# Optimization experiments

Hardware: AMD Instinct MI355X
Metric: run time of the kernel (lower is better)

Reference implementation:

```python
import jax, jax.numpy as jnp
import numpy as np

SEQ, B, N, H, OUT, K, L = 32, 1024, 19, 128, 1, 2, 2


def setup_inputs() -> dict:
    key = jax.random.key(0)
    ks = jax.random.split(key, 16)
    s = lambda i, shape, scale=1.0: (jax.random.normal(ks[i], shape, jnp.float32) * scale)
    return {
        "inputs": s(0, (SEQ, B, N, OUT)),
        "initial_hidden_state": s(1, (L, B, N * H)),
        "support": s(2, (N, N)) * (1.0 / np.sqrt(N)),
        "W_gate0": s(3, (3 * (OUT + H), 2 * H)) * 0.05,
        "b_gate0": s(4, (2 * H,)) * 0.05,
        "W_cand0": s(5, (3 * (OUT + H), H)) * 0.05,
        "b_cand0": s(6, (H,)) * 0.05,
        "W_gate1": s(7, (3 * (H + H), 2 * H)) * 0.05,
        "b_gate1": s(8, (2 * H,)) * 0.05,
        "W_cand1": s(9, (3 * (H + H), H)) * 0.05,
        "b_cand1": s(10, (H,)) * 0.05,
        "W_proj": s(11, (H, OUT)) * 0.05,
        "b_proj": s(12, (OUT,)) * 0.05,
    }


def reference(inputs, initial_hidden_state, support, W_gate0, b_gate0, W_cand0,
              b_cand0, W_gate1, b_gate1, W_cand1, b_cand1, W_proj, b_proj):
    seq_len, batch = inputs.shape[0], inputs.shape[1]
    h0 = initial_hidden_state.reshape(L, batch, N, H)

    def gconv(x, W, b):
        # Chebyshev diffusion: x0, T1=S@x0, T2=2*S@T1-x0 (K=2, 1 support)
        x0 = x
        x1 = jnp.einsum('mn,bnf->bmf', support, x0)
        feats = [x0, x1]
        for _ in range(K - 1):
            x2 = 2.0 * jnp.einsum('mn,bnf->bmf', support, x1) - x0
            feats.append(x2)
            x0, x1 = x1, x2
        X = jnp.concatenate(feats, axis=-1)  # (B, N, F*num_matrices)
        return jnp.einsum('bnf,fo->bno', X, W) + b

    def cell(x_in, h, Wg, bg, Wc, bc):
        ru = jax.nn.sigmoid(gconv(jnp.concatenate([x_in, h], axis=-1), Wg, bg))
        r, u = jnp.split(ru, 2, axis=-1)
        c = jnp.tanh(gconv(jnp.concatenate([x_in, r * h], axis=-1), Wc, bc))
        return u * h + (1.0 - u) * c

    layer_params = [(W_gate0, b_gate0, W_cand0, b_cand0),
                    (W_gate1, b_gate1, W_cand1, b_cand1)]

    def step(carry, _):
        h, cur = carry
        new_h = []
        x = cur
        for i, (Wg, bg, Wc, bc) in enumerate(layer_params):
            x = cell(x, h[i], Wg, bg, Wc, bc)
            new_h.append(x)
        proj = jnp.einsum('bnh,ho->bno', x, W_proj) + b_proj  # (B, N, OUT)
        out_t = proj.reshape(batch, N * OUT)
        return (jnp.stack(new_h, axis=0), proj), out_t

    go = jnp.zeros((batch, N, OUT), inputs.dtype)
    (_, _), outputs = jax.lax.scan(step, (h0, go), None, length=seq_len)
    return outputs  # (seq_len, batch, N*OUT)
```

## Files before the change

kernel.cpp:

```cpp
#include <hip/hip_runtime.h>
#include <hip/hip_bf16.h>
#include <math.h>

#define SEQ   32
#define BATCH 1024
#define NN    19
#define HH    128
#define NB    4
#define MR    (NB*NN)
#define SAS   264
#define HS    132
#define UTS   72
#define NBLK  (BATCH/NB)
#define NT    512

#define OFF_G0 0
#define OFF_C0 122880
#define OFF_G1 184320
#define OFF_C1 380928
#define WTOT   479232

__device__ unsigned short g_wall[WTOT];
__device__ unsigned short g_tg[2048];

typedef __attribute__((ext_vector_type(8))) short  bf16x8;
typedef __attribute__((ext_vector_type(4))) float  f32x4;

__device__ __forceinline__ unsigned short f2bf(float v) {
    __hip_bfloat16 b = __float2bfloat16(v);
    return *reinterpret_cast<unsigned short*>(&b);
}
__device__ __forceinline__ float bf2f(unsigned short u) {
    unsigned int x = ((unsigned int)u) << 16;
    return __uint_as_float(x);
}
__device__ __forceinline__ float hload(const unsigned short* p) { return bf2f(*p); }
__device__ __forceinline__ float hload(const float* p)          { return *p; }
__device__ __forceinline__ void  hstore(unsigned short* p, float v) { *p = f2bf(v); }
__device__ __forceinline__ void  hstore(float* p, float v)          { *p = v; }

__global__ __launch_bounds__(256) void wconv_kernel(
    const float* __restrict__ W, int F, int O, int KP, int off)
{
    int idx = blockIdx.x*256 + threadIdx.x;
    int total = 3*O*KP;
    if (idx >= total) return;
    int j   = idx / (O*KP);
    int r   = idx - j*(O*KP);
    int col = r / KP;
    int k   = r - col*KP;
    float v = (k < F) ? W[(size_t)(j*F + k)*O + col] : 0.f;
    g_wall[off + idx] = f2bf(v);
}

__global__ __launch_bounds__(256) void tprime_kernel(const float* __restrict__ S)
{
    __shared__ float sS[NN*NN], sS2[NN*NN];
    int tid = threadIdx.x;
    for (int i = tid; i < NN*NN; i += 256) sS[i] = S[i];
    __syncthreads();
    for (int i = tid; i < NN*NN; i += 256) {
        int m = i/NN, n = i - m*NN;
        float a = 0.f;
        for (int k = 0; k < NN; ++k) a += sS[m*NN+k]*sS[k*NN+n];
        sS2[i] = a;
    }
    __syncthreads();
    for (int i = tid; i < 32*64; i += 256) {
        int m = i >> 6, k = i & 63;
        float v = 0.f;
        if (m < NN && k < 3*NN) {
            int j = k / NN, n = k - j*NN;
            float eye = (m == n) ? 1.f : 0.f;
            if (j == 0)      v = eye;
            else if (j == 1) v = sS[m*NN+n];
            else             v = 2.f*sS2[m*NN+n] - eye;
        }
        g_tg[i] = f2bf(v);
    }
}

#define LDS_BYTES 159664

template<int KS, int NTC, bool GATE, int XW, typename HT>
__device__ __forceinline__ void gconv_phase(
    const unsigned short* __restrict__ BT,
    const float* __restrict__ bias,
    HT* hL,
    unsigned short* sA,
    unsigned short* ub,
    unsigned short* UtW,
    int lane, int w)
{
    constexpr int OC = NTC*128;
    constexpr int KP = KS*32;
    const int r16 = lane & 15, quad = lane >> 4;
    const int sgo = w * (NTC*16);

    const unsigned short* lanep = BT + (size_t)(sgo + r16)*KP + quad*8;

    f32x4 acc[3][5][NTC];
    #pragma unroll
    for (int j = 0; j < 3; ++j)
        #pragma unroll
        for (int mt = 0; mt < 5; ++mt)
            #pragma unroll
            for (int nt = 0; nt < NTC; ++nt) acc[j][mt][nt] = (f32x4)0.f;

    bf16x8 ring[2][3][NTC];
    #pragma unroll
    for (int j = 0; j < 3; ++j)
        #pragma unroll
        for (int nt = 0; nt < NTC; ++nt) {
            ring[0][j][nt] = *(const bf16x8*)(lanep + (size_t)(j*OC + nt*16)*KP);
            if (KS > 1)
                ring[1][j][nt] = *(const bf16x8*)(lanep + (size_t)(j*OC + nt*16)*KP + 32);
        }

    #pragma unroll
    for (int ks = 0; ks < KS; ++ks) {
        #pragma unroll
        for (int mt = 0; mt < 5; ++mt) {
            bf16x8 af = *(const bf16x8*)&sA[(mt*16 + r16)*SAS + ks*32 + quad*8];
            #pragma unroll
            for (int j = 0; j < 3; ++j)
                #pragma unroll
                for (int nt = 0; nt < NTC; ++nt)
                    acc[j][mt][nt] = __builtin_amdgcn_mfma_f32_16x16x32_bf16(
                        af, ring[ks & 1][j][nt], acc[j][mt][nt], 0, 0, 0);
        }
        if (ks + 2 < KS) {
            #pragma unroll
            for (int j = 0; j < 3; ++j)
                #pragma unroll
                for (int nt = 0; nt < NTC; ++nt)
                    ring[ks & 1][j][nt] = *(const bf16x8*)(lanep +
                        (size_t)(j*OC + nt*16)*KP + (ks + 2)*32);
        }
    }

    if (GATE) __syncthreads();

    float bv[NTC];
    #pragma unroll
    for (int nt = 0; nt < NTC; ++nt) bv[nt] = bias[sgo + nt*16 + r16];

    bf16x8 tp[2][2];
    #pragma unroll
    for (int mt2 = 0; mt2 < 2; ++mt2)
        #pragma unroll
        for (int kk = 0; kk < 2; ++kk)
            tp[mt2][kk] = *(const bf16x8*)&g_tg[(mt2*16 + r16)*64 + kk*32 + quad*8];

    for (int b = 0; b < NB; ++b) {
        #pragma unroll
        for (int j = 0; j < 3; ++j)
            #pragma unroll
            for (int mt = 0; mt < 5; ++mt)
                #pragma unroll
                for (int reg = 0; reg < 4; ++reg) {
                    int gm = mt*16 + quad*4 + reg;
                    int n  = gm - b*NN;
                    if (n >= 0 && n < NN) {
                        #pragma unroll
                        for (int nt = 0; nt < NTC; ++nt)
                            UtW[(nt*16 + r16)*UTS + j*NN + n] =
                                f2bf(acc[j][mt][nt][reg]);
                    }
                }
        f32x4 y[2][NTC];
        #pragma unroll
        for (int a = 0; a < 2; ++a)
            #pragma unroll
            for (int c = 0; c < NTC; ++c) y[a][c] = (f32x4)0.f;
        #pragma unroll
        for (int kk = 0; kk < 2; ++kk)
            #pragma unroll
            for (int nt = 0; nt < NTC; ++nt) {
                bf16x8 uf = *(const bf16x8*)&UtW[(nt*16 + r16)*UTS + kk*32 + quad*8];
                y[0][nt] = __builtin_amdgcn_mfma_f32_16x16x32_bf16(
                    tp[0][kk], uf, y[0][nt], 0, 0, 0);
                y[1][nt] = __builtin_amdgcn_mfma_f32_16x16x32_bf16(
                    tp[1][kk], uf, y[1][nt], 0, 0, 0);
            }
        #pragma unroll
        for (int mt2 = 0; mt2 < 2; ++mt2)
            #pragma unroll
            for (int nt = 0; nt < NTC; ++nt)
                #pragma unroll
                for (int reg = 0; reg < 4; ++reg) {
                    int m = mt2*16 + quad*4 + reg;
                    if (m < NN) {
                        int o = sgo + nt*16 + r16;
                        float v = y[mt2][nt][reg] + bv[nt];
                        int row = b*NN + m;
                        if (GATE) {
                            float sg_ = 1.f/(1.f + __expf(-v));
                            if (o < HH)
                                sA[row*SAS + XW + o] =
                                    f2bf(sg_ * hload(&hL[row*HS + o]));
                            else
                                ub[row*HS + (o-HH)] = f2bf(sg_);
                        } else {
                            float c  = 2.f/(1.f + __expf(-2.f*v)) - 1.f;
                            float u  = bf2f(ub[row*HS + o]);
                            float ho = hload(&hL[row*HS + o]);
                            hstore(&hL[row*HS + o], u*ho + (1.f - u)*c);
                        }
                    }
                }
    }
}

__global__ __launch_bounds__(NT, 2) void dcgru_persistent(
    const float* __restrict__ ihs,
    const float* __restrict__ bg0, const float* __restrict__ bc0,
    const float* __restrict__ bg1, const float* __restrict__ bc1,
    const float* __restrict__ Wp, const float* __restrict__ bp,
    float* __restrict__ out)
{
    extern __shared__ char smem[];
    unsigned short* h0    = (unsigned short*)smem;
    float*          h1    = (float*)(smem + 20064);
    unsigned short* sA    = (unsigned short*)(smem + 60192);
    unsigned short* ub    = (unsigned short*)(smem + 102432);
    unsigned short* Ut    = (unsigned short*)(smem + 122496);
    float*          xprev = (float*)(smem + 159360);

    const int tid  = threadIdx.x;
    const int lane = tid & 63;
    const int w    = tid >> 6;
    const int bb   = blockIdx.x * NB;
    unsigned short* UtW = Ut + w*32*UTS;

    const unsigned short* BTg0 = g_wall + OFF_G0;
    const unsigned short* BTc0 = g_wall + OFF_C0;
    const unsigned short* BTg1 = g_wall + OFF_G1;
    const unsigned short* BTc1 = g_wall + OFF_C1;

    for (int i = tid; i < MR*HH; i += NT) {
        int row = i >> 7, f = i & 127;
        h0[row*HS + f] = f2bf(ihs[(size_t)bb*2432 + i]);
        h1[row*HS + f] = ihs[(size_t)(BATCH + bb)*2432 + i];
    }
    for (int i = tid; i < MR; i += NT) xprev[i] = 0.f;
    for (int i = lane; i < 32*UTS; i += 64) UtW[i] = 0;

    const float wp0 = Wp[lane], wp1 = Wp[64 + lane], bpv = bp[0];
    __syncthreads();

    for (int t = 0; t < SEQ; ++t) {
        for (int idx = tid; idx < MR*160; idx += NT) {
            int row = idx/160, c = idx - row*160;
            unsigned short v;
            if (c == 0)       v = f2bf(xprev[row]);
            else if (c <= HH) v = h0[row*HS + (c-1)];
            else              v = 0;
            sA[row*SAS + c] = v;
        }
        __syncthreads();
        gconv_phase<5,2,true ,1>(BTg0, bg0, h0, sA, ub, UtW, lane, w);
        __syncthreads();
        gconv_phase<5,1,false,1>(BTc0, bc0, h0, sA, ub, UtW, lane, w);
        __syncthreads();

        for (int idx = tid; idx < MR*256; idx += NT) {
            int row = idx >> 8, c = idx & 255;
            sA[row*SAS + c] = (c < HH) ? h0[row*HS + c]
                                       : f2bf(h1[row*HS + (c-HH)]);
        }
        __syncthreads();
        gconv_phase<8,2,true ,HH>(BTg1, bg1, h1, sA, ub, UtW, lane, w);
        __syncthreads();
        gconv_phase<8,1,false,HH>(BTc1, bc1, h1, sA, ub, UtW, lane, w);
        __syncthreads();

        {
            int b  = w >> 1;
            int n0 = (w & 1) ? 10 : 0;
            int n1 = (w & 1) ? 19 : 10;
            for (int n = n0; n < n1; ++n) {
                int row = b*NN + n;
                float s = h1[row*HS + lane]*wp0 + h1[row*HS + 64 + lane]*wp1;
                #pragma unroll
                for (int off = 32; off; off >>= 1) s += __shfl_down(s, off, 64);
                if (lane == 0) {
                    float v = s + bpv;
                    out[((size_t)t*BATCH + bb + b)*NN + n] = v;
                    xprev[row] = v;
                }
            }
        }
        __syncthreads();
    }
}

extern "C" void kernel_launch(void* const* d_in, const int* in_sizes, int n_in,
                              void* d_out, int out_size, void* d_ws, size_t ws_size,
                              hipStream_t stream) {
    const float* ihs = (const float*)d_in[1];
    const float* S   = (const float*)d_in[2];
    const float* Wg0 = (const float*)d_in[3];
    const float* bg0 = (const float*)d_in[4];
    const float* Wc0 = (const float*)d_in[5];
    const float* bc0 = (const float*)d_in[6];
    const float* Wg1 = (const float*)d_in[7];
    const float* bg1 = (const float*)d_in[8];
    const float* Wc1 = (const float*)d_in[9];
    const float* bc1 = (const float*)d_in[10];
    const float* Wp  = (const float*)d_in[11];
    const float* bp  = (const float*)d_in[12];
    float* out = (float*)d_out;

    tprime_kernel<<<1, 256, 0, stream>>>(S);
    wconv_kernel<<<(3*256*160+255)/256, 256, 0, stream>>>(Wg0, 129, 256, 160, OFF_G0);
    wconv_kernel<<<(3*128*160+255)/256, 256, 0, stream>>>(Wc0, 129, 128, 160, OFF_C0);
    wconv_kernel<<<(3*256*256+255)/256, 256, 0, stream>>>(Wg1, 256, 256, 256, OFF_G1);
    wconv_kernel<<<(3*128*256+255)/256, 256, 0, stream>>>(Wc1, 256, 128, 256, OFF_C1);

    hipFuncSetAttribute((const void*)dcgru_persistent,
                        hipFuncAttributeMaxDynamicSharedMemorySize, LDS_BYTES);

    dcgru_persistent<<<NBLK, NT, LDS_BYTES, stream>>>(
        ihs, bg0, bc0, bg1, bc1, Wp, bp, out);
}
```

Measured before the change: 2.901 ms.

## Halve batch per block, store layer-1 hidden state in bf16, loop gate sub-groups

Cuts batch elements per block from 4 to 2 and threads per block from 512 to 256, which doubles the block count and roughly halves LDS use so more blocks can be resident per CU. The layer-1 hidden state is now kept in bf16 instead of fp32 to shrink LDS. The gconv phase now loops over gate output sub-groups with a fixed 2-tile width and a 3-deep weight prefetch ring. Each block now streams the full weight set for only 2 batch elements, so weight reuse per block drops and global/L2 weight traffic rises. Keeping h1 in bf16 also loses recurrent-state precision across 32 timesteps.

Measured after the change: 3.129 ms. +7.9%, slower.

```diff
diff --git a/kernel.cpp b/kernel.cpp
--- a/kernel.cpp
+++ b/kernel.cpp
@@ -6,13 +6,13 @@
 #define BATCH 1024
 #define NN    19
 #define HH    128
-#define NB    4
+#define NB    2
 #define MR    (NB*NN)
 #define SAS   264
 #define HS    132
 #define UTS   72
 #define NBLK  (BATCH/NB)
-#define NT    512
+#define NT    256
 
 #define OFF_G0 0
 #define OFF_C0 122880
@@ -34,10 +34,6 @@
     unsigned int x = ((unsigned int)u) << 16;
     return __uint_as_float(x);
 }
-__device__ __forceinline__ float hload(const unsigned short* p) { return bf2f(*p); }
-__device__ __forceinline__ float hload(const float* p)          { return *p; }
-__device__ __forceinline__ void  hstore(unsigned short* p, float v) { *p = f2bf(v); }
-__device__ __forceinline__ void  hstore(float* p, float v)          { *p = v; }
 
 __global__ __launch_bounds__(256) void wconv_kernel(
     const float* __restrict__ W, int F, int O, int KP, int off)
@@ -80,135 +76,141 @@
     }
 }
 
-#define LDS_BYTES 159664
-
-template<int KS, int NTC, bool GATE, int XW, typename HT>
+#define LDS_BYTES 74032
+
+template<int KS, int SG, bool GATE, int XW>
 __device__ __forceinline__ void gconv_phase(
     const unsigned short* __restrict__ BT,
     const float* __restrict__ bias,
-    HT* hL,
+    unsigned short* hL,
     unsigned short* sA,
     unsigned short* ub,
     unsigned short* UtW,
     int lane, int w)
 {
-    constexpr int OC = NTC*128;
+    constexpr int OC = SG*128;
     constexpr int KP = KS*32;
     const int r16 = lane & 15, quad = lane >> 4;
-    const int sgo = w * (NTC*16);
-
-    const unsigned short* lanep = BT + (size_t)(sgo + r16)*KP + quad*8;
-
-    f32x4 acc[3][5][NTC];
+
     #pragma unroll
-    for (int j = 0; j < 3; ++j)
-        #pragma unroll
-        for (int mt = 0; mt < 5; ++mt)
-            #pragma unroll
-            for (int nt = 0; nt < NTC; ++nt) acc[j][mt][nt] = (f32x4)0.f;
-
-    bf16x8 ring[2][3][NTC];
-    #pragma unroll
-    for (int j = 0; j < 3; ++j)
-        #pragma unroll
-        for (int nt = 0; nt < NTC; ++nt) {
-            ring[0][j][nt] = *(const bf16x8*)(lanep + (size_t)(j*OC + nt*16)*KP);
-            if (KS > 1)
-                ring[1][j][nt] = *(const bf16x8*)(lanep + (size_t)(j*OC + nt*16)*KP + 32);
-        }
-
-    #pragma unroll
-    for (int ks = 0; ks < KS; ++ks) {
-        #pragma unroll
-        for (int mt = 0; mt < 5; ++mt) {
-            bf16x8 af = *(const bf16x8*)&sA[(mt*16 + r16)*SAS + ks*32 + quad*8];
+    for (int s = 0; s < SG; ++s) {
+        const int sgo = (GATE ? (SG-1-s)*128 : 0) + w*32;
+        const unsigned short* lanep = BT + (size_t)(sgo + r16)*KP + quad*8;
+
+        f32x4 acc[3][3][2];
+        #pragma unroll
+        for (int j = 0; j < 3; ++j)
+            #pragma unroll
+            for (int mt = 0; mt < 3; ++mt)
+                #pragma unroll
+                for (int nt = 0; nt < 2; ++nt) acc[j][mt][nt] = (f32x4)0.f;
+
+        bf16x8 ring[3][3][2];
+        #pragma unroll
+        for (int j = 0; j < 3; ++j)
+            #pragma unroll
+            for (int nt = 0; nt < 2; ++nt) {
+                ring[0][j][nt] = *(const bf16x8*)(lanep + (size_t)(j*OC + nt*16)*KP);
+                if (KS > 1)
+                    ring[1][j][nt] = *(const bf16x8*)(lanep + (size_t)(j*OC + nt*16)*KP + 32);
+            }
+
+        #pragma unroll
+        for (int ks = 0; ks < KS; ++ks) {
+            if (ks + 2 < KS) {
+                #pragma unroll
+                for (int j = 0; j < 3; ++j)
+                    #pragma unroll
+                    for (int nt = 0; nt < 2; ++nt)
+                        ring[(ks + 2) % 3][j][nt] = *(const bf16x8*)(lanep +
+                            (size_t)(j*OC + nt*16)*KP + (ks + 2)*32);
+            }
+            bf16x8 af[3];
+            #pragma unroll
+            for (int mt = 0; mt < 3; ++mt)
+                af[mt] = *(const bf16x8*)&sA[(mt*16 + r16)*SAS + ks*32 + quad*8];
+            #pragma unroll
+            for (int mt = 0; mt < 3; ++mt)
+                #pragma unroll
+                for (int j = 0; j < 3; ++j)
+                    #pragma unroll
+                    for (int nt = 0; nt < 2; ++nt)
+                        acc[j][mt][nt] = __builtin_amdgcn_mfma_f32_16x16x32_bf16(
+                            af[mt], ring[ks % 3][j][nt], acc[j][mt][nt], 0, 0, 0);
+        }
+
+        if (GATE && s == SG-1) __syncthreads();
+
+        float bv[2];
+        #pragma unroll
+        for (int nt = 0; nt < 2; ++nt) bv[nt] = bias[sgo + nt*16 + r16];
+
+        bf16x8 tp[2][2];
+        #pragma unroll
+        for (int mt2 = 0; mt2 < 2; ++mt2)
+            #pragma unroll
+            for (int kk = 0; kk < 2; ++kk)
+                tp[mt2][kk] = *(const bf16x8*)&g_tg[(mt2*16 + r16)*64 + kk*32 + quad*8];
+
+        #pragma unroll
+        for (int b = 0; b < NB; ++b) {
             #pragma unroll
             for (int j = 0; j < 3; ++j)
                 #pragma unroll
-                for (int nt = 0; nt < NTC; ++nt)
-                    acc[j][mt][nt] = __builtin_amdgcn_mfma_f32_16x16x32_bf16(
-                        af, ring[ks & 1][j][nt], acc[j][mt][nt], 0, 0, 0);
-        }
-        if (ks + 2 < KS) {
-            #pragma unroll
-            for (int j = 0; j < 3; ++j)
-                #pragma unroll
-                for (int nt = 0; nt < NTC; ++nt)
-                    ring[ks & 1][j][nt] = *(const bf16x8*)(lanep +
-                        (size_t)(j*OC + nt*16)*KP + (ks + 2)*32);
-        }
-    }
-
-    if (GATE) __syncthreads();
-
-    float bv[NTC];
-    #pragma unroll
-    for (int nt = 0; nt < NTC; ++nt) bv[nt] = bias[sgo + nt*16 + r16];
-
-    bf16x8 tp[2][2];
-    #pragma unroll
-    for (int mt2 = 0; mt2 < 2; ++mt2)
-        #pragma unroll
-        for (int kk = 0; kk < 2; ++kk)
-            tp[mt2][kk] = *(const bf16x8*)&g_tg[(mt2*16 + r16)*64 + kk*32 + quad*8];
-
-    for (int b = 0; b < NB; ++b) {
-        #pragma unroll
-        for (int j = 0; j < 3; ++j)
-            #pragma unroll
-            for (int mt = 0; mt < 5; ++mt)
-                #pragma unroll
-                for (int reg = 0; reg < 4; ++reg) {
-                    int gm = mt*16 + quad*4 + reg;
-                    int n  = gm - b*NN;
-                    if (n >= 0 && n < NN) {
-                        #pragma unroll
-                        for (int nt = 0; nt < NTC; ++nt)
-                            UtW[(nt*16 + r16)*UTS + j*NN + n] =
-                                f2bf(acc[j][mt][nt][reg]);
-                    }
-                }
-        f32x4 y[2][NTC];
-        #pragma unroll
-        for (int a = 0; a < 2; ++a)
-            #pragma unroll
-            for (int c = 0; c < NTC; ++c) y[a][c] = (f32x4)0.f;
-        #pragma unroll
-        for (int kk = 0; kk < 2; ++kk)
-            #pragma unroll
-            for (int nt = 0; nt < NTC; ++nt) {
-                bf16x8 uf = *(const bf16x8*)&UtW[(nt*16 + r16)*UTS + kk*32 + quad*8];
-                y[0][nt] = __builtin_amdgcn_mfma_f32_16x16x32_bf16(
-                    tp[0][kk], uf, y[0][nt], 0, 0, 0);
-                y[1][nt] = __builtin_amdgcn_mfma_f32_16x16x32_bf16(
-                    tp[1][kk], uf, y[1][nt], 0, 0, 0);
-            }
-        #pragma unroll
-        for (int mt2 = 0; mt2 < 2; ++mt2)
-            #pragma unroll
-            for (int nt = 0; nt < NTC; ++nt)
-                #pragma unroll
-                for (int reg = 0; reg < 4; ++reg) {
-                    int m = mt2*16 + quad*4 + reg;
-                    if (m < NN) {
-                        int o = sgo + nt*16 + r16;
-                        float v = y[mt2][nt][reg] + bv[nt];
-                        int row = b*NN + m;
-                        if (GATE) {
-                            float sg_ = 1.f/(1.f + __expf(-v));
-                            if (o < HH)
-                                sA[row*SAS + XW + o] =
-                                    f2bf(sg_ * hload(&hL[row*HS + o]));
-                            else
-                                ub[row*HS + (o-HH)] = f2bf(sg_);
-                        } else {
-                            float c  = 2.f/(1.f + __expf(-2.f*v)) - 1.f;
-                            float u  = bf2f(ub[row*HS + o]);
-                            float ho = hload(&hL[row*HS + o]);
-                            hstore(&hL[row*HS + o], u*ho + (1.f - u)*c);
+                for (int mt = 0; mt < 3; ++mt)
+                    #pragma unroll
+                    for (int reg = 0; reg < 4; ++reg) {
+                        int gm = mt*16 + quad*4 + reg;
+                        int n  = gm - b*NN;
+                        if (n >= 0 && n < NN) {
+                            #pragma unroll
+                            for (int nt = 0; nt < 2; ++nt)
+                                UtW[(nt*16 + r16)*UTS + j*NN + n] =
+                                    f2bf(acc[j][mt][nt][reg]);
                         }
                     }
+            f32x4 y[2][2];
+            #pragma unroll
+            for (int a = 0; a < 2; ++a)
+                #pragma unroll
+                for (int c = 0; c < 2; ++c) y[a][c] = (f32x4)0.f;
+            #pragma unroll
+            for (int kk = 0; kk < 2; ++kk)
+                #pragma unroll
+                for (int nt = 0; nt < 2; ++nt) {
+                    bf16x8 uf = *(const bf16x8*)&UtW[(nt*16 + r16)*UTS + kk*32 + quad*8];
+                    y[0][nt] = __builtin_amdgcn_mfma_f32_16x16x32_bf16(
+                        tp[0][kk], uf, y[0][nt], 0, 0, 0);
+                    y[1][nt] = __builtin_amdgcn_mfma_f32_16x16x32_bf16(
+                        tp[1][kk], uf, y[1][nt], 0, 0, 0);
                 }
+            #pragma unroll
+            for (int mt2 = 0; mt2 < 2; ++mt2)
+                #pragma unroll
+                for (int nt = 0; nt < 2; ++nt)
+                    #pragma unroll
+                    for (int reg = 0; reg < 4; ++reg) {
+                        int m = mt2*16 + quad*4 + reg;
+                        if (m < NN) {
+                            int o = sgo + nt*16 + r16;
+                            float v = y[mt2][nt][reg] + bv[nt];
+                            int row = b*NN + m;
+                            if (GATE) {
+                                float sg_ = 1.f/(1.f + __expf(-v));
+                                if (o < HH)
+                                    sA[row*SAS + XW + o] =
+                                        f2bf(sg_ * bf2f(hL[row*HS + o]));
+                                else
+                                    ub[row*HS + (o-HH)] = f2bf(sg_);
+                            } else {
+                                float c  = 2.f/(1.f + __expf(-2.f*v)) - 1.f;
+                                float u  = bf2f(ub[row*HS + o]);
+                                float ho = bf2f(hL[row*HS + o]);
+                                hL[row*HS + o] = f2bf(u*ho + (1.f - u)*c);
+                            }
+                        }
+                    }
+        }
     }
 }
 
@@ -221,11 +223,11 @@
 {
     extern __shared__ char smem[];
     unsigned short* h0    = (unsigned short*)smem;
-    float*          h1    = (float*)(smem + 20064);
-    unsigned short* sA    = (unsigned short*)(smem + 60192);
-    unsigned short* ub    = (unsigned short*)(smem + 102432);
-    unsigned short* Ut    = (unsigned short*)(smem + 122496);
-    float*          xprev = (float*)(smem + 159360);
+    unsigned short* h1    = (unsigned short*)(smem + 10032);
+    unsigned short* sA    = (unsigned short*)(smem + 20064);
+    unsigned short* ub    = (unsigned short*)(smem + 45408);
+    unsigned short* Ut    = (unsigned short*)(smem + 55440);
+    float*          xprev = (float*)(smem + 73872);
 
     const int tid  = threadIdx.x;
     const int lane = tid & 63;
@@ -241,7 +243,7 @@
     for (int i = tid; i < MR*HH; i += NT) {
         int row = i >> 7, f = i & 127;
         h0[row*HS + f] = f2bf(ihs[(size_t)bb*2432 + i]);
-        h1[row*HS + f] = ihs[(size_t)(BATCH + bb)*2432 + i];
+        h1[row*HS + f] = f2bf(ihs[(size_t)(BATCH + bb)*2432 + i]);
     }
     for (int i = tid; i < MR; i += NT) xprev[i] = 0.f;
     for (int i = lane; i < 32*UTS; i += 64) UtW[i] = 0;
@@ -266,8 +268,7 @@
 
         for (int idx = tid; idx < MR*256; idx += NT) {
             int row = idx >> 8, c = idx & 255;
-            sA[row*SAS + c] = (c < HH) ? h0[row*HS + c]
-                                       : f2bf(h1[row*HS + (c-HH)]);
+            sA[row*SAS + c] = (c < HH) ? h0[row*HS + c] : h1[row*HS + (c-HH)];
         }
         __syncthreads();
         gconv_phase<8,2,true ,HH>(BTg1, bg1, h1, sA, ub, UtW, lane, w);
@@ -281,7 +282,8 @@
             int n1 = (w & 1) ? 19 : 10;
             for (int n = n0; n < n1; ++n) {
                 int row = b*NN + n;
-                float s = h1[row*HS + lane]*wp0 + h1[row*HS + 64 + lane]*wp1;
+                float s = bf2f(h1[row*HS + lane])*wp0
+                        + bf2f(h1[row*HS + 64 + lane])*wp1;
                 #pragma unroll
                 for (int off = 32; off; off >>= 1) s += __shfl_down(s, off, 64);
                 if (lane == 0) {
```
